# Optimization experiments

Measured on AMD Instinct MI355X. Metric: run time of the kernel, lower is better.

Reference implementation:

```python
import jax, jax.numpy as jnp
import numpy as np

H = 16          # num_attention_heads
HD = 64         # attention_head_size
ALPHA = 1.5
BANDWIDTH = 1.0
A_EXP = 0.5     # sinkhorn-like exponent 'a'
DIST_SCALE = float(HD)  # alpha < 2 => scale by head_size
EPS = 1e-12     # F.normalize eps


def setup_inputs() -> dict:
    key = jax.random.key(0)
    ks = jax.random.split(key, 5)
    B, L, D = 2, 1024, 1024
    w_scale = 0.02  # keep distances in a non-degenerate range for the power-law kernel
    x = jax.random.normal(ks[0], (B, L, D), dtype=jnp.float32)
    WQ = jax.random.normal(ks[1], (D, D), dtype=jnp.float32) * w_scale
    WK = jax.random.normal(ks[2], (D, D), dtype=jnp.float32) * w_scale
    WV = jax.random.normal(ks[3], (D, D), dtype=jnp.float32) * w_scale
    WO = jax.random.normal(ks[4], (D, D), dtype=jnp.float32) * w_scale
    z = jnp.zeros((D,), dtype=jnp.float32)
    return {"x": x, "WQ": WQ, "bQ": z, "WK": WK, "bK": z,
            "WV": WV, "bV": z, "WO": WO, "bO": z}


def _heads(t, B, L):
    # [B, L, H*HD] -> [B, H, L, HD]
    return t.reshape(B, L, H, HD).transpose(0, 2, 1, 3)


def reference(x, WQ, bQ, WK, bK, WV, bV, WO, bO):
    B, L, D = x.shape
    q = _heads(x @ WQ + bQ, B, L)   # [B,H,L,HD]
    k = _heads(x @ WK + bK, B, L)
    v = _heads(x @ WV + bV, B, L)

    # torch.cdist(q, k, p=2): pairwise euclidean distance [B,H,L,L]
    q2 = jnp.sum(q * q, axis=-1)                      # [B,H,L]
    k2 = jnp.sum(k * k, axis=-1)                      # [B,H,L]
    qk = jnp.einsum('bhid,bhjd->bhij', q, k)          # [B,H,L,L]
    d2 = q2[..., :, None] + k2[..., None, :] - 2.0 * qk
    g_dist = jnp.sqrt(jnp.maximum(d2, EPS)) / DIST_SCALE

    # alpha < 2: power-law kernel (1 + g/sqrt(bw))^(-(d_intrinsic + alpha))
    attn_score = (1.0 + g_dist / np.sqrt(BANDWIDTH)) ** (-(HD + ALPHA))

    # a > 0: Sinkhorn-style row/col renormalization
    N_R = jnp.sum(attn_score, axis=-1)                # [B,H,L] row sums
    N_C = jnp.sum(attn_score, axis=-2)                # [B,H,L] col sums
    K_tilde = (N_R ** (-A_EXP))[..., :, None] * attn_score * (N_C ** (-A_EXP))[..., None, :]

    # F.normalize(p=1, dim=3); entries are positive so |.| sum == sum
    attention_probs = K_tilde / jnp.maximum(jnp.sum(K_tilde, axis=-1, keepdims=True), EPS)

    out = jnp.einsum('bhij,bhjd->bhid', attention_probs, v)   # [B,H,L,HD]
    out = out.transpose(0, 2, 1, 3).reshape(B, L, H * HD)
    return out @ WO + bO
```

## Files before the change

### kernel.cpp

```cpp
#include <hip/hip_runtime.h>
#include <math.h>


typedef __attribute__((ext_vector_type(8))) short short8;
typedef __attribute__((ext_vector_type(4))) float f32x4;

__device__ inline unsigned short f2bf(float f) {
  unsigned int u = __float_as_uint(f);
  unsigned int r = (u + 0x7FFFu + ((u >> 16) & 1u)) >> 16;
  return (unsigned short)r;
}
__device__ inline float bf2f(unsigned short s) {
  return __uint_as_float(((unsigned int)s) << 16);
}
__device__ inline float score_fn(float dot, float sq) {
  float d2 = fmaxf(fmaf(-2.f, dot, sq), 1e-12f);
  float sd = __builtin_amdgcn_sqrtf(d2);
  float lg = __builtin_amdgcn_logf(fmaf(sd, 0.015625f, 1.0f));
  return __builtin_amdgcn_exp2f(-65.5f * lg);
}
__device__ inline unsigned int cvtpk(float lo, float hi) {
  unsigned int r;
  asm("v_cvt_pk_bf16_f32 %0, %1, %2" : "=v"(r) : "v"(lo), "v"(hi));
  return r;
}
#define GLD16(lptr, gptr)                                                      \
  __builtin_amdgcn_global_load_lds(                                            \
      (const __attribute__((address_space(1))) void*)(gptr),                   \
      (__attribute__((address_space(3))) void*)(lptr), 16, 0, 0)

__global__ __launch_bounds__(256) void prep(const float* __restrict__ x,
                                            unsigned short* __restrict__ xb,
                                            const float* __restrict__ W0,
                                            const float* __restrict__ W1,
                                            const float* __restrict__ W2,
                                            const float* __restrict__ W3,
                                            unsigned short* __restrict__ T0,
                                            unsigned short* __restrict__ T1,
                                            unsigned short* __restrict__ T2,
                                            unsigned short* __restrict__ T3) {
  __shared__ float T[32][33];
  int bx = blockIdx.x;
  if (bx < 2048) {
    int i = bx * 256 + threadIdx.x;
    float4 v = ((const float4*)x)[i];
    xb[4 * i + 0] = f2bf(v.x);
    xb[4 * i + 1] = f2bf(v.y);
    xb[4 * i + 2] = f2bf(v.z);
    xb[4 * i + 3] = f2bf(v.w);
    return;
  }
  int idx = bx - 2048;
  int z = idx >> 10, rem = idx & 1023;
  const float* W = z == 0 ? W0 : z == 1 ? W1 : z == 2 ? W2 : W3;
  unsigned short* WT = z == 0 ? T0 : z == 1 ? T1 : z == 2 ? T2 : T3;
  int k0 = (rem >> 5) * 32, n0 = (rem & 31) * 32;
  int c = threadIdx.x & 31, r8 = threadIdx.x >> 5;
#pragma unroll
  for (int it = 0; it < 4; ++it) {
    int rr = r8 + it * 8;
    T[rr][c] = W[(size_t)(k0 + rr) * 1024 + n0 + c];
  }
  __syncthreads();
#pragma unroll
  for (int it = 0; it < 4; ++it) {
    int rr = r8 + it * 8;
    WT[(size_t)(n0 + rr) * 1024 + k0 + c] = f2bf(T[c][rr]);
  }
}

__global__ __launch_bounds__(512, 2) void gemm128k64(const unsigned short* __restrict__ A,
                                                     const unsigned short* __restrict__ B0,
                                                     const unsigned short* __restrict__ B1,
                                                     const unsigned short* __restrict__ B2,
                                                     const float* __restrict__ c0,
                                                     const float* __restrict__ c1,
                                                     const float* __restrict__ c2,
                                                     void* __restrict__ Y0,
                                                     void* __restrict__ Y1,
                                                     void* __restrict__ Y2,
                                                     float* __restrict__ sq0,
                                                     float* __restrict__ sq1,
                                                     float* __restrict__ sq2,
                                                     int m0, int m1, int m2) {
  int z = blockIdx.z;
  const unsigned short* BT = z == 0 ? B0 : z == 1 ? B1 : B2;
  const float* bias = z == 0 ? c0 : z == 1 ? c1 : c2;
  void* Y = z == 0 ? Y0 : z == 1 ? Y1 : Y2;
  float* sq = z == 0 ? sq0 : z == 1 ? sq1 : sq2;
  int mode = z == 0 ? m0 : z == 1 ? m1 : m2;

  __shared__ __align__(16) unsigned short As[2][128 * 64];
  __shared__ __align__(16) unsigned short Bs[2][128 * 64];
  int tid = threadIdx.x;
  int w = tid >> 6, l = tid & 63, g = l >> 4, l15 = l & 15;
  int wm = w >> 2, wn = w & 3;
  int bm = blockIdx.x * 128, bn = blockIdx.y * 128;
  const int x7 = l15 & 7;

  const int i0 = tid, i1 = tid + 512;
  const int r0 = i0 >> 3, s0 = (i0 & 7) ^ (r0 & 7);
  const int r1 = i1 >> 3, s1 = (i1 & 7) ^ (r1 & 7);

  GLD16(&As[0][i0 * 8], &A[(size_t)(bm + r0) * 1024 + s0 * 8]);
  GLD16(&As[0][i1 * 8], &A[(size_t)(bm + r1) * 1024 + s1 * 8]);
  GLD16(&Bs[0][i0 * 8], &BT[(size_t)(bn + r0) * 1024 + s0 * 8]);
  GLD16(&Bs[0][i1 * 8], &BT[(size_t)(bn + r1) * 1024 + s1 * 8]);

  f32x4 acc[4][2];
#pragma unroll
  for (int mi = 0; mi < 4; ++mi)
#pragma unroll
    for (int ni = 0; ni < 2; ++ni)
#pragma unroll
      for (int r = 0; r < 4; ++r) acc[mi][ni][r] = 0.f;

  __syncthreads();
  for (int t = 0; t < 16; ++t) {
    int cur = t & 1;
    if (t < 15) {
      int kn = (t + 1) * 64;
      GLD16(&As[cur ^ 1][i0 * 8], &A[(size_t)(bm + r0) * 1024 + kn + s0 * 8]);
      GLD16(&As[cur ^ 1][i1 * 8], &A[(size_t)(bm + r1) * 1024 + kn + s1 * 8]);
      GLD16(&Bs[cur ^ 1][i0 * 8], &BT[(size_t)(bn + r0) * 1024 + kn + s0 * 8]);
      GLD16(&Bs[cur ^ 1][i1 * 8], &BT[(size_t)(bn + r1) * 1024 + kn + s1 * 8]);
    }
#pragma unroll
    for (int kc = 0; kc < 2; ++kc) {
      const int cread = (((kc << 2) + g) ^ x7) * 8;
      short8 a[4], b[2];
#pragma unroll
      for (int mi = 0; mi < 4; ++mi)
        a[mi] = *(const short8*)&As[cur][(wm * 64 + mi * 16 + l15) * 64 + cread];
#pragma unroll
      for (int ni = 0; ni < 2; ++ni)
        b[ni] = *(const short8*)&Bs[cur][(wn * 32 + ni * 16 + l15) * 64 + cread];
#pragma unroll
      for (int mi = 0; mi < 4; ++mi)
#pragma unroll
        for (int ni = 0; ni < 2; ++ni)
          acc[mi][ni] = __builtin_amdgcn_mfma_f32_16x16x32_bf16(a[mi], b[ni], acc[mi][ni], 0, 0, 0);
    }
    __syncthreads();
  }

  float rowsq[4][4];
#pragma unroll
  for (int mi = 0; mi < 4; ++mi)
#pragma unroll
    for (int r = 0; r < 4; ++r) rowsq[mi][r] = 0.f;

#pragma unroll
  for (int ni = 0; ni < 2; ++ni) {
    int n = bn + wn * 32 + ni * 16 + l15;
    float bv = bias[n];
#pragma unroll
    for (int mi = 0; mi < 4; ++mi) {
#pragma unroll
      for (int r = 0; r < 4; ++r) {
        int m = bm + wm * 64 + mi * 16 + 4 * g + r;
        float v = acc[mi][ni][r] + bv;
        if (mode == 0) {
          int b = m >> 10, ll = m & 1023, h = n >> 6, hd = n & 63;
          unsigned short ush = f2bf(v);
          ((unsigned short*)Y)[(((size_t)(b * 16 + h) * 1024) + ll) * 64 + hd] = ush;
          float f = bf2f(ush);
          rowsq[mi][r] = fmaf(f, f, rowsq[mi][r]);
        } else if (mode == 1) {
          int b = m >> 10, ll = m & 1023, h = n >> 6, hd = n & 63;
          int jp = (ll & ~31) | (((ll >> 2) & 3) * 8 + ((ll >> 4) & 1) * 4 + (ll & 3));
          ((unsigned short*)Y)[(((size_t)(b * 16 + h) * 64) + hd) * 1024 + jp] = f2bf(v);
        } else {
          ((float*)Y)[(size_t)m * 1024 + n] = v;
        }
      }
    }
  }

  if (sq != nullptr) {
    float* Sq = (float*)&As[0][0];
#pragma unroll
    for (int mi = 0; mi < 4; ++mi)
#pragma unroll
      for (int r = 0; r < 4; ++r) {
        float s = rowsq[mi][r];
        s += __shfl_xor(s, 1);
        s += __shfl_xor(s, 2);
        s += __shfl_xor(s, 4);
        s += __shfl_xor(s, 8);
        rowsq[mi][r] = s;
      }
    if (l15 == 0) {
#pragma unroll
      for (int mi = 0; mi < 4; ++mi)
#pragma unroll
        for (int r = 0; r < 4; ++r)
          Sq[(wm * 4 + wn) * 64 + mi * 16 + 4 * g + r] = rowsq[mi][r];
    }
    __syncthreads();
    if (tid < 256) {
      int rr = tid & 127, hh = tid >> 7;
      float s = Sq[((rr >> 6) * 4 + 2 * hh) * 64 + (rr & 63)] +
                Sq[((rr >> 6) * 4 + 2 * hh + 1) * 64 + (rr & 63)];
      int m = bm + rr, b = m >> 10, ll = m & 1023;
      int h = (bn >> 6) + hh;
      sq[(size_t)(b * 16 + h) * 1024 + ll] = s;
    }
  }
}

__global__ __launch_bounds__(256) void gemm_st(const unsigned short* __restrict__ A,
                                               const unsigned short* __restrict__ BT,
                                               const float* __restrict__ bias,
                                               float* __restrict__ Y) {
  __shared__ __align__(16) unsigned short As[2][64 * 64];
  __shared__ __align__(16) unsigned short Bs[2][64 * 64];
  int tid = threadIdx.x;
  int w = tid >> 6, l = tid & 63, g = l >> 4, l15 = l & 15;
  int bm = blockIdx.x * 64, bn = blockIdx.y * 64;
  const int arow = w * 16 + l15;
  const int x7 = l15 & 7;

  const int i0s = tid, i1s = 256 + tid;
  const int r0 = i0s >> 3, s0 = (i0s & 7) ^ (r0 & 7);
  const int r1 = i1s >> 3, s1 = (i1s & 7) ^ (r1 & 7);

  GLD16(&As[0][i0s * 8], &A[(size_t)(bm + r0) * 1024 + s0 * 8]);
  GLD16(&As[0][i1s * 8], &A[(size_t)(bm + r1) * 1024 + s1 * 8]);
  GLD16(&Bs[0][i0s * 8], &BT[(size_t)(bn + r0) * 1024 + s0 * 8]);
  GLD16(&Bs[0][i1s * 8], &BT[(size_t)(bn + r1) * 1024 + s1 * 8]);

  f32x4 acc[4];
#pragma unroll
  for (int t = 0; t < 4; ++t)
#pragma unroll
    for (int r = 0; r < 4; ++r) acc[t][r] = 0.f;

  __syncthreads();
  for (int t = 0; t < 16; ++t) {
    int cur = t & 1;
    if (t < 15) {
      int kn = (t + 1) * 64;
      GLD16(&As[cur ^ 1][i0s * 8], &A[(size_t)(bm + r0) * 1024 + kn + s0 * 8]);
      GLD16(&As[cur ^ 1][i1s * 8], &A[(size_t)(bm + r1) * 1024 + kn + s1 * 8]);
      GLD16(&Bs[cur ^ 1][i0s * 8], &BT[(size_t)(bn + r0) * 1024 + kn + s0 * 8]);
      GLD16(&Bs[cur ^ 1][i1s * 8], &BT[(size_t)(bn + r1) * 1024 + kn + s1 * 8]);
    }
#pragma unroll
    for (int kc = 0; kc < 2; ++kc) {
      short8 a = *(const short8*)&As[cur][arow * 64 + ((kc * 4 + g) ^ x7) * 8];
#pragma unroll
      for (int tt = 0; tt < 4; ++tt) {
        short8 b = *(const short8*)&Bs[cur][(tt * 16 + l15) * 64 + ((kc * 4 + g) ^ x7) * 8];
        acc[tt] = __builtin_amdgcn_mfma_f32_16x16x32_bf16(a, b, acc[tt], 0, 0, 0);
      }
    }
    __syncthreads();
  }

#pragma unroll
  for (int t = 0; t < 4; ++t) {
    int n = bn + 16 * t + l15;
    float bv = bias[n];
#pragma unroll
    for (int r = 0; r < 4; ++r) {
      int m = bm + w * 16 + 4 * g + r;
      Y[(size_t)m * 1024 + n] = acc[t][r] + bv;
    }
  }
}

__global__ __launch_bounds__(256, 2) void colsum_mfma(const unsigned short* __restrict__ Qb,
                                                      const unsigned short* __restrict__ Kb,
                                                      const float* __restrict__ q2,
                                                      const float* __restrict__ k2,
                                                      float* __restrict__ rnc) {
  __shared__ __align__(16) unsigned short Qd[2][128 * 64];
  __shared__ __align__(16) float q2s[1024];
  int bh = blockIdx.x, jt = blockIdx.y;
  int tid = threadIdx.x, w = tid >> 6, l = tid & 63;
  int g = l >> 4, l15 = l & 15;
  const int x7 = l15 & 7;
  const unsigned short* Qp = Qb + (size_t)bh * 65536;
  const unsigned short* Kp = Kb + (size_t)bh * 65536;
  int j = jt * 64 + w * 16 + l15;

  int rQ[4], sQ[4];
#pragma unroll
  for (int it = 0; it < 4; ++it) {
    int c = tid + 256 * it;
    rQ[it] = c >> 3;
    sQ[it] = (c & 7) ^ (rQ[it] & 7);
  }

  GLD16(&q2s[tid * 4], q2 + (size_t)bh * 1024 + tid * 4);
#pragma unroll
  for (int it = 0; it < 4; ++it)
    GLD16(&Qd[0][(tid + 256 * it) * 8], Qp + (size_t)rQ[it] * 64 + sQ[it] * 8);

  short8 bk0 = *(const short8*)&Kp[(size_t)j * 64 + 8 * g];
  short8 bk1 = *(const short8*)&Kp[(size_t)j * 64 + 32 + 8 * g];
  float k2j = k2[(size_t)bh * 1024 + j];
  float colacc = 0.f;

  __syncthreads();
  for (int t = 0; t < 8; ++t) {
    int cur = t & 1;
    if (t < 7) {
      int inx = (t + 1) * 128;
#pragma unroll
      for (int it = 0; it < 4; ++it)
        GLD16(&Qd[cur ^ 1][(tid + 256 * it) * 8], Qp + (size_t)(inx + rQ[it]) * 64 + sQ[it] * 8);
    }
    const unsigned short* Ql = Qd[cur];
#pragma unroll
    for (int tp = 0; tp < 8; ++tp) {
      int rowb = (16 * tp + l15) * 64;
      short8 a0 = *(const short8*)&Ql[rowb + ((g) ^ x7) * 8];
      short8 a1 = *(const short8*)&Ql[rowb + ((4 + g) ^ x7) * 8];
      f32x4 cf;
#pragma unroll
      for (int r = 0; r < 4; ++r) cf[r] = 0.f;
      __builtin_amdgcn_s_setprio(1);
      cf = __builtin_amdgcn_mfma_f32_16x16x32_bf16(a0, bk0, cf, 0, 0, 0);
      cf = __builtin_amdgcn_mfma_f32_16x16x32_bf16(a1, bk1, cf, 0, 0, 0);
      __builtin_amdgcn_s_setprio(0);
      float4 qv = *(const float4*)&q2s[t * 128 + 16 * tp + 4 * g];
      colacc += score_fn(cf[0], qv.x + k2j);
      colacc += score_fn(cf[1], qv.y + k2j);
      colacc += score_fn(cf[2], qv.z + k2j);
      colacc += score_fn(cf[3], qv.w + k2j);
    }
    __syncthreads();
  }
  colacc += __shfl_xor(colacc, 16);
  colacc += __shfl_xor(colacc, 32);
  if (l < 16) rnc[(size_t)bh * 1024 + jt * 64 + w * 16 + l] = __builtin_amdgcn_rsqf(colacc);
}

__global__ __launch_bounds__(256, 2) void attn_mfma(const unsigned short* __restrict__ Qb,
                                                    const unsigned short* __restrict__ Kb,
                                                    const unsigned short* __restrict__ VTp,
                                                    const float* __restrict__ q2,
                                                    const float* __restrict__ k2,
                                                    const float* __restrict__ rnc,
                                                    unsigned short* __restrict__ AO) {
  __shared__ __align__(16) unsigned short Kd[2][128 * 64];
  __shared__ __align__(16) unsigned short Vd[2][64 * 128];
  __shared__ __align__(16) float k2s[1024];
  __shared__ __align__(16) float rns[1024];
  int bh = blockIdx.x;
  int tid = threadIdx.x, w = tid >> 6, l = tid & 63;
  int g = l >> 4, l15 = l & 15;
  const int x7 = l15 & 7;
  int it0 = blockIdx.y * 64 + w * 16;
  const unsigned short* Qp = Qb + (size_t)bh * 65536;
  const unsigned short* Kp = Kb + (size_t)bh * 65536;
  const unsigned short* Vp = VTp + (size_t)bh * 65536;
  int b = bh >> 4, h = bh & 15;

  int rK[4], cK[4], rV[4], cV[4];
#pragma unroll
  for (int it = 0; it < 4; ++it) {
    int c = tid + 256 * it;
    rK[it] = c >> 3;
    cK[it] = ((c & 7) ^ (rK[it] & 7));
    rV[it] = c >> 4;
    int s = c & 15;
    cV[it] = (s & 8) | ((s & 7) ^ (rV[it] & 7));
  }

  GLD16(&k2s[tid * 4], k2 + (size_t)bh * 1024 + tid * 4);
  GLD16(&rns[tid * 4], rnc + (size_t)bh * 1024 + tid * 4);
#pragma unroll
  for (int it = 0; it < 4; ++it) {
    GLD16(&Kd[0][(tid + 256 * it) * 8], Kp + (size_t)rK[it] * 64 + cK[it] * 8);
    GLD16(&Vd[0][(tid + 256 * it) * 8], Vp + (size_t)rV[it] * 1024 + cV[it] * 8);
  }

  short8 bq0 = *(const short8*)&Qp[(size_t)(it0 + l15) * 64 + 8 * g];
  short8 bq1 = *(const short8*)&Qp[(size_t)(it0 + l15) * 64 + 32 + 8 * g];
  float q2l = q2[(size_t)bh * 1024 + it0 + l15];

  f32x4 o[4];
#pragma unroll
  for (int t = 0; t < 4; ++t)
#pragma unroll
    for (int r = 0; r < 4; ++r) o[t][r] = 0.f;
  float dacc = 0.f;

  __syncthreads();
  for (int t = 0; t < 8; ++t) {
    int cur = t & 1;
    if (t < 7) {
      int j0n = (t + 1) * 128;
#pragma unroll
      for (int it = 0; it < 4; ++it) {
        GLD16(&Kd[cur ^ 1][(tid + 256 * it) * 8], Kp + (size_t)(j0n + rK[it]) * 64 + cK[it] * 8);
        GLD16(&Vd[cur ^ 1][(tid + 256 * it) * 8], Vp + (size_t)rV[it] * 1024 + j0n + cV[it] * 8);
      }
    }
    const unsigned short* Kl = Kd[cur];
    const unsigned short* Vl = Vd[cur];
#pragma unroll
    for (int jj = 0; jj < 2; ++jj) {
      float sc[16];
#pragma unroll
      for (int tp = 0; tp < 4; ++tp) {
        int rowb = (jj * 64 + 16 * tp + l15) * 64;
        short8 a0 = *(const short8*)&Kl[rowb + ((g) ^ x7) * 8];
        short8 a1 = *(const short8*)&Kl[rowb + ((4 + g) ^ x7) * 8];
        f32x4 cf;
#pragma unroll
        for (int r = 0; r < 4; ++r) cf[r] = 0.f;
        __builtin_amdgcn_s_setprio(1);
        cf = __builtin_amdgcn_mfma_f32_16x16x32_bf16(a0, bq0, cf, 0, 0, 0);
        cf = __builtin_amdgcn_mfma_f32_16x16x32_bf16(a1, bq1, cf, 0, 0, 0);
        __builtin_amdgcn_s_setprio(0);
        int base = t * 128 + jj * 64 + 16 * tp + 4 * g;
        float4 kv = *(const float4*)&k2s[base];
        float4 rv = *(const float4*)&rns[base];
        sc[tp * 4 + 0] = score_fn(cf[0], q2l + kv.x) * rv.x;
        sc[tp * 4 + 1] = score_fn(cf[1], q2l + kv.y) * rv.y;
        sc[tp * 4 + 2] = score_fn(cf[2], q2l + kv.z) * rv.z;
        sc[tp * 4 + 3] = score_fn(cf[3], q2l + kv.w) * rv.w;
      }
#pragma unroll
      for (int i = 0; i < 16; ++i) dacc += sc[i];
      int pi0[4], pi1[4];
      pi0[0] = (int)cvtpk(sc[0], sc[1]);
      pi0[1] = (int)cvtpk(sc[2], sc[3]);
      pi0[2] = (int)cvtpk(sc[4], sc[5]);
      pi0[3] = (int)cvtpk(sc[6], sc[7]);
      pi1[0] = (int)cvtpk(sc[8], sc[9]);
      pi1[1] = (int)cvtpk(sc[10], sc[11]);
      pi1[2] = (int)cvtpk(sc[12], sc[13]);
      pi1[3] = (int)cvtpk(sc[14], sc[15]);
      short8 pa0 = *(short8*)pi0;
      short8 pa1 = *(short8*)pi1;
#pragma unroll
      for (int t5 = 0; t5 < 4; ++t5) {
        int vr = 16 * t5 + l15;
        short8 bv0 = *(const short8*)&Vl[vr * 128 + (jj * 8 + ((g) ^ x7)) * 8];
        short8 bv1 = *(const short8*)&Vl[vr * 128 + (jj * 8 + ((4 + g) ^ x7)) * 8];
        __builtin_amdgcn_s_setprio(1);
        o[t5] = __builtin_amdgcn_mfma_f32_16x16x32_bf16(pa0, bv0, o[t5], 0, 0, 0);
        o[t5] = __builtin_amdgcn_mfma_f32_16x16x32_bf16(pa1, bv1, o[t5], 0, 0, 0);
        __builtin_amdgcn_s_setprio(0);
      }
    }
    __syncthreads();
  }

  dacc += __shfl_xor(dacc, 16);
  dacc += __shfl_xor(dacc, 32);
  float dv[4];
#pragma unroll
  for (int r = 0; r < 4; ++r) dv[r] = __shfl(dacc, 4 * g + r);

#pragma unroll
  for (int t = 0; t < 4; ++t) {
#pragma unroll
    for (int r = 0; r < 4; ++r) {
      int m = b * 1024 + it0 + 4 * g + r;
      int n = h * 64 + t * 16 + l15;
      AO[(size_t)m * 1024 + n] = f2bf(o[t][r] / dv[r]);
    }
  }
}

extern "C" void kernel_launch(void* const* d_in, const int* in_sizes, int n_in,
                              void* d_out, int out_size, void* d_ws, size_t ws_size,
                              hipStream_t stream) {
  const float* x  = (const float*)d_in[0];
  const float* WQ = (const float*)d_in[1];
  const float* bQ = (const float*)d_in[2];
  const float* WK = (const float*)d_in[3];
  const float* bK = (const float*)d_in[4];
  const float* WV = (const float*)d_in[5];
  const float* bV = (const float*)d_in[6];
  const float* WO = (const float*)d_in[7];
  const float* bO = (const float*)d_in[8];

  char* base = (char*)d_ws;
  unsigned short* xb  = (unsigned short*)(base);
  unsigned short* WQT = (unsigned short*)(base + (4u  << 20));
  unsigned short* WKT = (unsigned short*)(base + (6u  << 20));
  unsigned short* WVT = (unsigned short*)(base + (8u  << 20));
  unsigned short* WOT = (unsigned short*)(base + (10u << 20));
  unsigned short* Qb  = (unsigned short*)(base + (12u << 20));
  unsigned short* Kb  = (unsigned short*)(base + (16u << 20));
  unsigned short* VTp = (unsigned short*)(base + (20u << 20));
  unsigned short* AOb = (unsigned short*)(base + (24u << 20));
  float* q2  = (float*)(base + (28u << 20));
  float* k2  = (float*)(base + (28u << 20) + (128u << 10));
  float* rnc = (float*)(base + (28u << 20) + (256u << 10));

  prep<<<6144, 256, 0, stream>>>(x, xb, WQ, WK, WV, WO, WQT, WKT, WVT, WOT);

  gemm128k64<<<dim3(16, 8, 3), 512, 0, stream>>>(xb, WQT, WKT, WVT, bQ, bK, bV,
                                                 Qb, Kb, VTp, q2, k2, nullptr,
                                                 0, 0, 1);

  colsum_mfma<<<dim3(32, 16), 256, 0, stream>>>(Qb, Kb, q2, k2, rnc);
  attn_mfma<<<dim3(32, 16), 256, 0, stream>>>(Qb, Kb, VTp, q2, k2, rnc, AOb);

  gemm_st<<<dim3(32, 16), 256, 0, stream>>>(AOb, WOT, bO, (float*)d_out);
}
```

Baseline: 98.72 us.

## Split colsum and attention over the key/query dimension with a combine pass

The column-sum and attention kernels are each split in two along the reduction dimension (grid z=2), so twice as many blocks run with smaller LDS tiles and a higher occupancy hint. Partial column sums are added and turned into inverse square roots inside the attention kernel. Partial outputs and row denominators go to fp32 workspace, and a new combine kernel sums them, normalizes and writes bf16. The aim is to fill the 256 CUs better than 512 blocks could, at the cost of an extra launch and extra global traffic for the fp32 partials.

```diff
diff --git a/kernel.cpp b/kernel.cpp
--- a/kernel.cpp
+++ b/kernel.cpp
@@ -270,33 +270,29 @@
   }
 }
 
-__global__ __launch_bounds__(256, 2) void colsum_mfma(const unsigned short* __restrict__ Qb,
+__global__ __launch_bounds__(256, 4) void colsum_part(const unsigned short* __restrict__ Qb,
                                                       const unsigned short* __restrict__ Kb,
                                                       const float* __restrict__ q2,
                                                       const float* __restrict__ k2,
-                                                      float* __restrict__ rnc) {
-  __shared__ __align__(16) unsigned short Qd[2][128 * 64];
-  __shared__ __align__(16) float q2s[1024];
-  int bh = blockIdx.x, jt = blockIdx.y;
+                                                      float* __restrict__ ncp) {
+  __shared__ __align__(16) unsigned short Qd[2][64 * 64];
+  __shared__ __align__(16) float q2s[512];
+  int bh = blockIdx.x, jt = blockIdx.y, ih = blockIdx.z;
   int tid = threadIdx.x, w = tid >> 6, l = tid & 63;
   int g = l >> 4, l15 = l & 15;
   const int x7 = l15 & 7;
   const unsigned short* Qp = Qb + (size_t)bh * 65536;
   const unsigned short* Kp = Kb + (size_t)bh * 65536;
+  const int ibase = ih * 512;
   int j = jt * 64 + w * 16 + l15;
 
-  int rQ[4], sQ[4];
-#pragma unroll
-  for (int it = 0; it < 4; ++it) {
-    int c = tid + 256 * it;
-    rQ[it] = c >> 3;
-    sQ[it] = (c & 7) ^ (rQ[it] & 7);
-  }
-
-  GLD16(&q2s[tid * 4], q2 + (size_t)bh * 1024 + tid * 4);
-#pragma unroll
-  for (int it = 0; it < 4; ++it)
-    GLD16(&Qd[0][(tid + 256 * it) * 8], Qp + (size_t)rQ[it] * 64 + sQ[it] * 8);
+  const int i0s = tid, i1s = 256 + tid;
+  const int r0 = i0s >> 3, s0 = (i0s & 7) ^ (r0 & 7);
+  const int r1 = i1s >> 3, s1 = (i1s & 7) ^ (r1 & 7);
+
+  if (tid < 128) GLD16(&q2s[tid * 4], q2 + (size_t)bh * 1024 + ibase + tid * 4);
+  GLD16(&Qd[0][i0s * 8], Qp + (size_t)(ibase + r0) * 64 + s0 * 8);
+  GLD16(&Qd[0][i1s * 8], Qp + (size_t)(ibase + r1) * 64 + s1 * 8);
 
   short8 bk0 = *(const short8*)&Kp[(size_t)j * 64 + 8 * g];
   short8 bk1 = *(const short8*)&Kp[(size_t)j * 64 + 32 + 8 * g];
@@ -307,14 +303,13 @@
   for (int t = 0; t < 8; ++t) {
     int cur = t & 1;
     if (t < 7) {
-      int inx = (t + 1) * 128;
-#pragma unroll
-      for (int it = 0; it < 4; ++it)
-        GLD16(&Qd[cur ^ 1][(tid + 256 * it) * 8], Qp + (size_t)(inx + rQ[it]) * 64 + sQ[it] * 8);
+      int inx = ibase + (t + 1) * 64;
+      GLD16(&Qd[cur ^ 1][i0s * 8], Qp + (size_t)(inx + r0) * 64 + s0 * 8);
+      GLD16(&Qd[cur ^ 1][i1s * 8], Qp + (size_t)(inx + r1) * 64 + s1 * 8);
     }
     const unsigned short* Ql = Qd[cur];
 #pragma unroll
-    for (int tp = 0; tp < 8; ++tp) {
+    for (int tp = 0; tp < 4; ++tp) {
       int rowb = (16 * tp + l15) * 64;
       short8 a0 = *(const short8*)&Ql[rowb + ((g) ^ x7) * 8];
       short8 a1 = *(const short8*)&Ql[rowb + ((4 + g) ^ x7) * 8];
@@ -325,7 +320,7 @@
       cf = __builtin_amdgcn_mfma_f32_16x16x32_bf16(a0, bk0, cf, 0, 0, 0);
       cf = __builtin_amdgcn_mfma_f32_16x16x32_bf16(a1, bk1, cf, 0, 0, 0);
       __builtin_amdgcn_s_setprio(0);
-      float4 qv = *(const float4*)&q2s[t * 128 + 16 * tp + 4 * g];
+      float4 qv = *(const float4*)&q2s[t * 64 + 16 * tp + 4 * g];
       colacc += score_fn(cf[0], qv.x + k2j);
       colacc += score_fn(cf[1], qv.y + k2j);
       colacc += score_fn(cf[2], qv.z + k2j);
@@ -335,48 +330,50 @@
   }
   colacc += __shfl_xor(colacc, 16);
   colacc += __shfl_xor(colacc, 32);
-  if (l < 16) rnc[(size_t)bh * 1024 + jt * 64 + w * 16 + l] = __builtin_amdgcn_rsqf(colacc);
-}
-
-__global__ __launch_bounds__(256, 2) void attn_mfma(const unsigned short* __restrict__ Qb,
+  if (l < 16)
+    ncp[(size_t)(ih * 32 + bh) * 1024 + jt * 64 + w * 16 + l] = colacc;
+}
+
+__global__ __launch_bounds__(256, 4) void attn_part(const unsigned short* __restrict__ Qb,
                                                     const unsigned short* __restrict__ Kb,
                                                     const unsigned short* __restrict__ VTp,
                                                     const float* __restrict__ q2,
                                                     const float* __restrict__ k2,
-                                                    const float* __restrict__ rnc,
-                                                    unsigned short* __restrict__ AO) {
-  __shared__ __align__(16) unsigned short Kd[2][128 * 64];
-  __shared__ __align__(16) unsigned short Vd[2][64 * 128];
-  __shared__ __align__(16) float k2s[1024];
-  __shared__ __align__(16) float rns[1024];
-  int bh = blockIdx.x;
+                                                    const float* __restrict__ ncp,
+                                                    float* __restrict__ Opart,
+                                                    float* __restrict__ dpart) {
+  __shared__ __align__(16) unsigned short Kd[2][64 * 64];
+  __shared__ __align__(16) unsigned short Vd[2][64 * 64];
+  __shared__ __align__(16) float k2s[512];
+  __shared__ __align__(16) float rns[512];
+  int bh = blockIdx.x, it = blockIdx.y, jh = blockIdx.z;
   int tid = threadIdx.x, w = tid >> 6, l = tid & 63;
   int g = l >> 4, l15 = l & 15;
   const int x7 = l15 & 7;
-  int it0 = blockIdx.y * 64 + w * 16;
+  int it0 = it * 64 + w * 16;
+  const int jg = jh * 512;
   const unsigned short* Qp = Qb + (size_t)bh * 65536;
   const unsigned short* Kp = Kb + (size_t)bh * 65536;
   const unsigned short* Vp = VTp + (size_t)bh * 65536;
-  int b = bh >> 4, h = bh & 15;
-
-  int rK[4], cK[4], rV[4], cV[4];
-#pragma unroll
-  for (int it = 0; it < 4; ++it) {
-    int c = tid + 256 * it;
-    rK[it] = c >> 3;
-    cK[it] = ((c & 7) ^ (rK[it] & 7));
-    rV[it] = c >> 4;
-    int s = c & 15;
-    cV[it] = (s & 8) | ((s & 7) ^ (rV[it] & 7));
-  }
-
-  GLD16(&k2s[tid * 4], k2 + (size_t)bh * 1024 + tid * 4);
-  GLD16(&rns[tid * 4], rnc + (size_t)bh * 1024 + tid * 4);
-#pragma unroll
-  for (int it = 0; it < 4; ++it) {
-    GLD16(&Kd[0][(tid + 256 * it) * 8], Kp + (size_t)rK[it] * 64 + cK[it] * 8);
-    GLD16(&Vd[0][(tid + 256 * it) * 8], Vp + (size_t)rV[it] * 1024 + cV[it] * 8);
-  }
+
+  {
+    float2 a0 = *(const float2*)&ncp[(size_t)bh * 1024 + jg + tid * 2];
+    float2 a1 = *(const float2*)&ncp[(size_t)(32 + bh) * 1024 + jg + tid * 2];
+    rns[tid * 2 + 0] = __builtin_amdgcn_rsqf(a0.x + a1.x);
+    rns[tid * 2 + 1] = __builtin_amdgcn_rsqf(a0.y + a1.y);
+    float2 kk = *(const float2*)&k2[(size_t)bh * 1024 + jg + tid * 2];
+    k2s[tid * 2 + 0] = kk.x;
+    k2s[tid * 2 + 1] = kk.y;
+  }
+
+  const int i0s = tid, i1s = 256 + tid;
+  const int r0 = i0s >> 3, s0 = (i0s & 7) ^ (r0 & 7);
+  const int r1 = i1s >> 3, s1 = (i1s & 7) ^ (r1 & 7);
+
+  GLD16(&Kd[0][i0s * 8], Kp + (size_t)(jg + r0) * 64 + s0 * 8);
+  GLD16(&Kd[0][i1s * 8], Kp + (size_t)(jg + r1) * 64 + s1 * 8);
+  GLD16(&Vd[0][i0s * 8], Vp + (size_t)r0 * 1024 + jg + s0 * 8);
+  GLD16(&Vd[0][i1s * 8], Vp + (size_t)r1 * 1024 + jg + s1 * 8);
 
   short8 bq0 = *(const short8*)&Qp[(size_t)(it0 + l15) * 64 + 8 * g];
   short8 bq1 = *(const short8*)&Qp[(size_t)(it0 + l15) * 64 + 32 + 8 * g];
@@ -393,79 +390,106 @@
   for (int t = 0; t < 8; ++t) {
     int cur = t & 1;
     if (t < 7) {
-      int j0n = (t + 1) * 128;
-#pragma unroll
-      for (int it = 0; it < 4; ++it) {
-        GLD16(&Kd[cur ^ 1][(tid + 256 * it) * 8], Kp + (size_t)(j0n + rK[it]) * 64 + cK[it] * 8);
-        GLD16(&Vd[cur ^ 1][(tid + 256 * it) * 8], Vp + (size_t)rV[it] * 1024 + j0n + cV[it] * 8);
-      }
+      int j0n = jg + (t + 1) * 64;
+      GLD16(&Kd[cur ^ 1][i0s * 8], Kp + (size_t)(j0n + r0) * 64 + s0 * 8);
+      GLD16(&Kd[cur ^ 1][i1s * 8], Kp + (size_t)(j0n + r1) * 64 + s1 * 8);
+      GLD16(&Vd[cur ^ 1][i0s * 8], Vp + (size_t)r0 * 1024 + j0n + s0 * 8);
+      GLD16(&Vd[cur ^ 1][i1s * 8], Vp + (size_t)r1 * 1024 + j0n + s1 * 8);
     }
     const unsigned short* Kl = Kd[cur];
     const unsigned short* Vl = Vd[cur];
-#pragma unroll
-    for (int jj = 0; jj < 2; ++jj) {
-      float sc[16];
-#pragma unroll
-      for (int tp = 0; tp < 4; ++tp) {
-        int rowb = (jj * 64 + 16 * tp + l15) * 64;
-        short8 a0 = *(const short8*)&Kl[rowb + ((g) ^ x7) * 8];
-        short8 a1 = *(const short8*)&Kl[rowb + ((4 + g) ^ x7) * 8];
-        f32x4 cf;
-#pragma unroll
-        for (int r = 0; r < 4; ++r) cf[r] = 0.f;
-        __builtin_amdgcn_s_setprio(1);
-        cf = __builtin_amdgcn_mfma_f32_16x16x32_bf16(a0, bq0, cf, 0, 0, 0);
-        cf = __builtin_amdgcn_mfma_f32_16x16x32_bf16(a1, bq1, cf, 0, 0, 0);
-        __builtin_amdgcn_s_setprio(0);
-        int base = t * 128 + jj * 64 + 16 * tp + 4 * g;
-        float4 kv = *(const float4*)&k2s[base];
-        float4 rv = *(const float4*)&rns[base];
-        sc[tp * 4 + 0] = score_fn(cf[0], q2l + kv.x) * rv.x;
-        sc[tp * 4 + 1] = score_fn(cf[1], q2l + kv.y) * rv.y;
-        sc[tp * 4 + 2] = score_fn(cf[2], q2l + kv.z) * rv.z;
-        sc[tp * 4 + 3] = score_fn(cf[3], q2l + kv.w) * rv.w;
-      }
-#pragma unroll
-      for (int i = 0; i < 16; ++i) dacc += sc[i];
-      int pi0[4], pi1[4];
-      pi0[0] = (int)cvtpk(sc[0], sc[1]);
-      pi0[1] = (int)cvtpk(sc[2], sc[3]);
-      pi0[2] = (int)cvtpk(sc[4], sc[5]);
-      pi0[3] = (int)cvtpk(sc[6], sc[7]);
-      pi1[0] = (int)cvtpk(sc[8], sc[9]);
-      pi1[1] = (int)cvtpk(sc[10], sc[11]);
-      pi1[2] = (int)cvtpk(sc[12], sc[13]);
-      pi1[3] = (int)cvtpk(sc[14], sc[15]);
-      short8 pa0 = *(short8*)pi0;
-      short8 pa1 = *(short8*)pi1;
-#pragma unroll
-      for (int t5 = 0; t5 < 4; ++t5) {
-        int vr = 16 * t5 + l15;
-        short8 bv0 = *(const short8*)&Vl[vr * 128 + (jj * 8 + ((g) ^ x7)) * 8];
-        short8 bv1 = *(const short8*)&Vl[vr * 128 + (jj * 8 + ((4 + g) ^ x7)) * 8];
-        __builtin_amdgcn_s_setprio(1);
-        o[t5] = __builtin_amdgcn_mfma_f32_16x16x32_bf16(pa0, bv0, o[t5], 0, 0, 0);
-        o[t5] = __builtin_amdgcn_mfma_f32_16x16x32_bf16(pa1, bv1, o[t5], 0, 0, 0);
-        __builtin_amdgcn_s_setprio(0);
-      }
+    float sc[16];
+#pragma unroll
+    for (int tp = 0; tp < 4; ++tp) {
+      int rowb = (16 * tp + l15) * 64;
+      short8 a0 = *(const short8*)&Kl[rowb + ((g) ^ x7) * 8];
+      short8 a1 = *(const short8*)&Kl[rowb + ((4 + g) ^ x7) * 8];
+      f32x4 cf;
+#pragma unroll
+      for (int r = 0; r < 4; ++r) cf[r] = 0.f;
+      __builtin_amdgcn_s_setprio(1);
+      cf = __builtin_amdgcn_mfma_f32_16x16x32_bf16(a0, bq0, cf, 0, 0, 0);
+      cf = __builtin_amdgcn_mfma_f32_16x16x32_bf16(a1, bq1, cf, 0, 0, 0);
+      __builtin_amdgcn_s_setprio(0);
+      int base = t * 64 + 16 * tp + 4 * g;
+      float4 kv = *(const float4*)&k2s[base];
+      float4 rv = *(const float4*)&rns[base];
+      sc[tp * 4 + 0] = score_fn(cf[0], q2l + kv.x) * rv.x;
+      sc[tp * 4 + 1] = score_fn(cf[1], q2l + kv.y) * rv.y;
+      sc[tp * 4 + 2] = score_fn(cf[2], q2l + kv.z) * rv.z;
+      sc[tp * 4 + 3] = score_fn(cf[3], q2l + kv.w) * rv.w;
+    }
+#pragma unroll
+    for (int i = 0; i < 16; ++i) dacc += sc[i];
+    int pi0[4], pi1[4];
+    pi0[0] = (int)cvtpk(sc[0], sc[1]);
+    pi0[1] = (int)cvtpk(sc[2], sc[3]);
+    pi0[2] = (int)cvtpk(sc[4], sc[5]);
+    pi0[3] = (int)cvtpk(sc[6], sc[7]);
+    pi1[0] = (int)cvtpk(sc[8], sc[9]);
+    pi1[1] = (int)cvtpk(sc[10], sc[11]);
+    pi1[2] = (int)cvtpk(sc[12], sc[13]);
+    pi1[3] = (int)cvtpk(sc[14], sc[15]);
+    short8 pa0 = *(short8*)pi0;
+    short8 pa1 = *(short8*)pi1;
+#pragma unroll
+    for (int t5 = 0; t5 < 4; ++t5) {
+      int rowb = (16 * t5 + l15) * 64;
+      short8 v0 = *(const short8*)&Vl[rowb + ((g) ^ x7) * 8];
+      short8 v1 = *(const short8*)&Vl[rowb + ((4 + g) ^ x7) * 8];
+      __builtin_amdgcn_s_setprio(1);
+      o[t5] = __builtin_amdgcn_mfma_f32_16x16x32_bf16(pa0, v0, o[t5], 0, 0, 0);
+      o[t5] = __builtin_amdgcn_mfma_f32_16x16x32_bf16(pa1, v1, o[t5], 0, 0, 0);
+      __builtin_amdgcn_s_setprio(0);
     }
     __syncthreads();
   }
 
   dacc += __shfl_xor(dacc, 16);
   dacc += __shfl_xor(dacc, 32);
-  float dv[4];
-#pragma unroll
-  for (int r = 0; r < 4; ++r) dv[r] = __shfl(dacc, 4 * g + r);
-
-#pragma unroll
-  for (int t = 0; t < 4; ++t) {
+  if (l < 16)
+    dpart[(size_t)(jh * 32 + bh) * 1024 + it * 64 + w * 16 + l] = dacc;
+
+  float* Ob = Opart + ((size_t)(jh * 32 + bh) * 16 + it) * 4096;
+#pragma unroll
+  for (int t5 = 0; t5 < 4; ++t5) {
 #pragma unroll
     for (int r = 0; r < 4; ++r) {
-      int m = b * 1024 + it0 + 4 * g + r;
-      int n = h * 64 + t * 16 + l15;
-      AO[(size_t)m * 1024 + n] = f2bf(o[t][r] / dv[r]);
-    }
+      int ri = w * 16 + 4 * g + r;
+      int ci = 16 * t5 + l15;
+      Ob[ri * 64 + ci] = o[t5][r];
+    }
+  }
+}
+
+__global__ __launch_bounds__(256) void combine(const float* __restrict__ Opart,
+                                               const float* __restrict__ dpart,
+                                               unsigned short* __restrict__ AO) {
+  __shared__ float dl[64];
+  int bh = blockIdx.x, it = blockIdx.y;
+  int tid = threadIdx.x;
+  int b = bh >> 4, h = bh & 15;
+  const float* O0 = Opart + ((size_t)bh * 16 + it) * 4096;
+  const float* O1 = Opart + ((size_t)(32 + bh) * 16 + it) * 4096;
+  if (tid < 64)
+    dl[tid] = dpart[(size_t)bh * 1024 + it * 64 + tid] +
+              dpart[(size_t)(32 + bh) * 1024 + it * 64 + tid];
+  __syncthreads();
+#pragma unroll
+  for (int e = 0; e < 4; ++e) {
+    int idx = (tid + e * 256) * 4;
+    int ri = idx >> 6, ci = idx & 63;
+    float4 a = *(const float4*)&O0[idx];
+    float4 c = *(const float4*)&O1[idx];
+    float inv = 1.0f / dl[ri];
+    unsigned short outv[4];
+    outv[0] = f2bf((a.x + c.x) * inv);
+    outv[1] = f2bf((a.y + c.y) * inv);
+    outv[2] = f2bf((a.z + c.z) * inv);
+    outv[3] = f2bf((a.w + c.w) * inv);
+    int m = b * 1024 + it * 64 + ri;
+    int n = h * 64 + ci;
+    *(unsigned long long*)&AO[(size_t)m * 1024 + n] = *(unsigned long long*)outv;
   }
 }
 
@@ -492,9 +516,11 @@
   unsigned short* Kb  = (unsigned short*)(base + (16u << 20));
   unsigned short* VTp = (unsigned short*)(base + (20u << 20));
   unsigned short* AOb = (unsigned short*)(base + (24u << 20));
-  float* q2  = (float*)(base + (28u << 20));
-  float* k2  = (float*)(base + (28u << 20) + (128u << 10));
-  float* rnc = (float*)(base + (28u << 20) + (256u << 10));
+  float* q2    = (float*)(base + (28u << 20));
+  float* k2    = (float*)(base + (28u << 20) + (128u << 10));
+  float* ncp   = (float*)(base + (29u << 20));
+  float* dpart = (float*)(base + (30u << 20));
+  float* Opart = (float*)(base + (31u << 20));
 
   prep<<<6144, 256, 0, stream>>>(x, xb, WQ, WK, WV, WO, WQT, WKT, WVT, WOT);
 
@@ -502,8 +528,10 @@
                                                  Qb, Kb, VTp, q2, k2, nullptr,
                                                  0, 0, 1);
 
-  colsum_mfma<<<dim3(32, 16), 256, 0, stream>>>(Qb, Kb, q2, k2, rnc);
-  attn_mfma<<<dim3(32, 16), 256, 0, stream>>>(Qb, Kb, VTp, q2, k2, rnc, AOb);
+  colsum_part<<<dim3(32, 16, 2), 256, 0, stream>>>(Qb, Kb, q2, k2, ncp);
+  attn_part<<<dim3(32, 16, 2), 256, 0, stream>>>(Qb, Kb, VTp, q2, k2, ncp,
+                                                 Opart, dpart);
+  combine<<<dim3(32, 16), 256, 0, stream>>>(Opart, dpart, AOb);
 
   gemm_st<<<dim3(32, 16), 256, 0, stream>>>(AOb, WOT, bO, (float*)d_out);
 }
```

Result: slower. 102.2 us (+3.5%).

## Materialize score matrix once and fold column normalization into scaled V

Applied to the files above, without the earlier changes.

Before, the power-law score matrix was computed twice: once to get column sums and again inside the attention kernel. Now a first pass computes the scores once, writes them as a bf16 matrix P to global memory, and accumulates column sums. A small kernel then scales V by the inverse square root of those sums and appends a row of those factors, so the P·V pass also yields the row denominators. This removes the duplicate transcendental work but adds about 64 MB of P writes and reads plus an extra launch, and the column scaling is now applied after bf16 rounding of the unscaled scores.

```diff
diff --git a/kernel.cpp b/kernel.cpp
--- a/kernel.cpp
+++ b/kernel.cpp
@@ -270,201 +270,215 @@
   }
 }
 
-__global__ __launch_bounds__(256, 2) void colsum_mfma(const unsigned short* __restrict__ Qb,
-                                                      const unsigned short* __restrict__ Kb,
-                                                      const float* __restrict__ q2,
-                                                      const float* __restrict__ k2,
-                                                      float* __restrict__ rnc) {
-  __shared__ __align__(16) unsigned short Qd[2][128 * 64];
+__global__ __launch_bounds__(256, 4) void passA(const unsigned short* __restrict__ Qb,
+                                                const unsigned short* __restrict__ Kb,
+                                                const float* __restrict__ q2,
+                                                const float* __restrict__ k2,
+                                                unsigned short* __restrict__ P,
+                                                float* __restrict__ rnc) {
+  __shared__ __align__(16) unsigned short Qd[2][64 * 64];
   __shared__ __align__(16) float q2s[1024];
+  __shared__ __align__(16) unsigned int Pb[2][64][36];
+  __shared__ float colred[4][64];
   int bh = blockIdx.x, jt = blockIdx.y;
   int tid = threadIdx.x, w = tid >> 6, l = tid & 63;
   int g = l >> 4, l15 = l & 15;
   const int x7 = l15 & 7;
   const unsigned short* Qp = Qb + (size_t)bh * 65536;
   const unsigned short* Kp = Kb + (size_t)bh * 65536;
-  int j = jt * 64 + w * 16 + l15;
-
-  int rQ[4], sQ[4];
-#pragma unroll
-  for (int it = 0; it < 4; ++it) {
-    int c = tid + 256 * it;
-    rQ[it] = c >> 3;
-    sQ[it] = (c & 7) ^ (rQ[it] & 7);
-  }
+
+  const int i0s = tid, i1s = 256 + tid;
+  const int r0 = i0s >> 3, s0 = (i0s & 7) ^ (r0 & 7);
+  const int r1 = i1s >> 3, s1 = (i1s & 7) ^ (r1 & 7);
 
   GLD16(&q2s[tid * 4], q2 + (size_t)bh * 1024 + tid * 4);
-#pragma unroll
-  for (int it = 0; it < 4; ++it)
-    GLD16(&Qd[0][(tid + 256 * it) * 8], Qp + (size_t)rQ[it] * 64 + sQ[it] * 8);
-
-  short8 bk0 = *(const short8*)&Kp[(size_t)j * 64 + 8 * g];
-  short8 bk1 = *(const short8*)&Kp[(size_t)j * 64 + 32 + 8 * g];
-  float k2j = k2[(size_t)bh * 1024 + j];
-  float colacc = 0.f;
+  GLD16(&Qd[0][i0s * 8], Qp + (size_t)r0 * 64 + s0 * 8);
+  GLD16(&Qd[0][i1s * 8], Qp + (size_t)r1 * 64 + s1 * 8);
+
+  short8 ak[4][2];
+#pragma unroll
+  for (int tp = 0; tp < 4; ++tp) {
+#pragma unroll
+    for (int hf = 0; hf < 2; ++hf)
+      ak[tp][hf] = *(const short8*)&Kp[(size_t)(jt * 64 + 16 * tp + l15) * 64 + hf * 32 + 8 * g];
+  }
+  float k2v[16];
+#pragma unroll
+  for (int tp = 0; tp < 4; ++tp) {
+    float4 kk = *(const float4*)&k2[(size_t)bh * 1024 + jt * 64 + 16 * tp + 4 * g];
+    k2v[tp * 4 + 0] = kk.x; k2v[tp * 4 + 1] = kk.y;
+    k2v[tp * 4 + 2] = kk.z; k2v[tp * 4 + 3] = kk.w;
+  }
+  float colpart[16];
+#pragma unroll
+  for (int q = 0; q < 16; ++q) colpart[q] = 0.f;
+
+  const int iloc = w * 16 + l15;
+  const int pr0 = tid >> 3, pc0 = tid & 7;
+  const int pr1 = (tid + 256) >> 3, pc1 = tid & 7;
 
   __syncthreads();
-  for (int t = 0; t < 8; ++t) {
+  for (int t = 0; t < 16; ++t) {
     int cur = t & 1;
-    if (t < 7) {
-      int inx = (t + 1) * 128;
-#pragma unroll
-      for (int it = 0; it < 4; ++it)
-        GLD16(&Qd[cur ^ 1][(tid + 256 * it) * 8], Qp + (size_t)(inx + rQ[it]) * 64 + sQ[it] * 8);
-    }
-    const unsigned short* Ql = Qd[cur];
-#pragma unroll
-    for (int tp = 0; tp < 8; ++tp) {
-      int rowb = (16 * tp + l15) * 64;
-      short8 a0 = *(const short8*)&Ql[rowb + ((g) ^ x7) * 8];
-      short8 a1 = *(const short8*)&Ql[rowb + ((4 + g) ^ x7) * 8];
+    if (t < 15) {
+      int inx = (t + 1) * 64;
+      GLD16(&Qd[cur ^ 1][i0s * 8], Qp + (size_t)(inx + r0) * 64 + s0 * 8);
+      GLD16(&Qd[cur ^ 1][i1s * 8], Qp + (size_t)(inx + r1) * 64 + s1 * 8);
+    }
+    int rowb = iloc * 64;
+    short8 bq0 = *(const short8*)&Qd[cur][rowb + ((g) ^ x7) * 8];
+    short8 bq1 = *(const short8*)&Qd[cur][rowb + ((4 + g) ^ x7) * 8];
+    float q2l = q2s[t * 64 + iloc];
+
+    float sc[16];
+#pragma unroll
+    for (int tp = 0; tp < 4; ++tp) {
       f32x4 cf;
 #pragma unroll
       for (int r = 0; r < 4; ++r) cf[r] = 0.f;
-      __builtin_amdgcn_s_setprio(1);
-      cf = __builtin_amdgcn_mfma_f32_16x16x32_bf16(a0, bk0, cf, 0, 0, 0);
-      cf = __builtin_amdgcn_mfma_f32_16x16x32_bf16(a1, bk1, cf, 0, 0, 0);
-      __builtin_amdgcn_s_setprio(0);
-      float4 qv = *(const float4*)&q2s[t * 128 + 16 * tp + 4 * g];
-      colacc += score_fn(cf[0], qv.x + k2j);
-      colacc += score_fn(cf[1], qv.y + k2j);
-      colacc += score_fn(cf[2], qv.z + k2j);
-      colacc += score_fn(cf[3], qv.w + k2j);
+      cf = __builtin_amdgcn_mfma_f32_16x16x32_bf16(ak[tp][0], bq0, cf, 0, 0, 0);
+      cf = __builtin_amdgcn_mfma_f32_16x16x32_bf16(ak[tp][1], bq1, cf, 0, 0, 0);
+#pragma unroll
+      for (int r = 0; r < 4; ++r)
+        sc[tp * 4 + r] = score_fn(cf[r], q2l + k2v[tp * 4 + r]);
+    }
+#pragma unroll
+    for (int q = 0; q < 16; ++q) colpart[q] += sc[q];
+
+#pragma unroll
+    for (int tp = 0; tp < 4; ++tp) {
+#pragma unroll
+      for (int rp = 0; rp < 2; ++rp) {
+        int dwidx = 16 * (tp >> 1) + 4 * g + 2 * (tp & 1) + rp;
+        Pb[cur][iloc][dwidx] = cvtpk(sc[tp * 4 + 2 * rp], sc[tp * 4 + 2 * rp + 1]);
+      }
     }
     __syncthreads();
-  }
-  colacc += __shfl_xor(colacc, 16);
-  colacc += __shfl_xor(colacc, 32);
-  if (l < 16) rnc[(size_t)bh * 1024 + jt * 64 + w * 16 + l] = __builtin_amdgcn_rsqf(colacc);
-}
-
-__global__ __launch_bounds__(256, 2) void attn_mfma(const unsigned short* __restrict__ Qb,
-                                                    const unsigned short* __restrict__ Kb,
-                                                    const unsigned short* __restrict__ VTp,
-                                                    const float* __restrict__ q2,
-                                                    const float* __restrict__ k2,
-                                                    const float* __restrict__ rnc,
-                                                    unsigned short* __restrict__ AO) {
-  __shared__ __align__(16) unsigned short Kd[2][128 * 64];
-  __shared__ __align__(16) unsigned short Vd[2][64 * 128];
-  __shared__ __align__(16) float k2s[1024];
-  __shared__ __align__(16) float rns[1024];
-  int bh = blockIdx.x;
+    {
+      short8 v0 = *(const short8*)((const char*)&Pb[cur][0][0] + 144 * pr0 + 16 * pc0);
+      short8 v1 = *(const short8*)((const char*)&Pb[cur][0][0] + 144 * pr1 + 16 * pc1);
+      *(short8*)&P[((size_t)bh * 1024 + t * 64 + pr0) * 1024 + jt * 64 + 8 * pc0] = v0;
+      *(short8*)&P[((size_t)bh * 1024 + t * 64 + pr1) * 1024 + jt * 64 + 8 * pc1] = v1;
+    }
+  }
+
+#pragma unroll
+  for (int q = 0; q < 16; ++q) {
+    float v = colpart[q];
+    v += __shfl_xor(v, 1);
+    v += __shfl_xor(v, 2);
+    v += __shfl_xor(v, 4);
+    v += __shfl_xor(v, 8);
+    colpart[q] = v;
+  }
+  if (l15 == 0) {
+#pragma unroll
+    for (int q = 0; q < 16; ++q)
+      colred[w][16 * (q >> 2) + 4 * g + (q & 3)] = colpart[q];
+  }
+  __syncthreads();
+  if (tid < 64) {
+    float s = colred[0][tid] + colred[1][tid] + colred[2][tid] + colred[3][tid];
+    rnc[(size_t)bh * 1024 + jt * 64 + tid] = __builtin_amdgcn_rsqf(s);
+  }
+}
+
+__global__ __launch_bounds__(256) void vscale(const unsigned short* __restrict__ VTp,
+                                              const float* __restrict__ rnc,
+                                              unsigned short* __restrict__ Vs) {
+  int bh = blockIdx.x, row = blockIdx.y;
+  int j4 = threadIdx.x * 4;
+  unsigned short out[4];
+#pragma unroll
+  for (int e = 0; e < 4; ++e) {
+    int jp = j4 + e;
+    int p = jp & 31;
+    int gg = (p >> 3) & 3, jj = (p >> 2) & 1, rr = p & 3;
+    int jtrue = (jp & ~31) | (16 * jj + 4 * gg + rr);
+    float rv = rnc[(size_t)bh * 1024 + jtrue];
+    if (row < 64) {
+      float v = bf2f(VTp[((size_t)bh * 64 + row) * 1024 + jp]);
+      out[e] = f2bf(v * rv);
+    } else if (row == 64) {
+      out[e] = f2bf(rv);
+    } else {
+      out[e] = 0;
+    }
+  }
+  *(unsigned long long*)&Vs[((size_t)bh * 80 + row) * 1024 + j4] = *(unsigned long long*)out;
+}
+
+__global__ __launch_bounds__(256, 4) void passB(const unsigned short* __restrict__ P,
+                                                const unsigned short* __restrict__ Vs,
+                                                unsigned short* __restrict__ AO) {
+  __shared__ __align__(16) unsigned short Pd[2][64 * 64];
+  __shared__ __align__(16) unsigned short Vd[2][80 * 64];
+  int bh = blockIdx.x, it = blockIdx.y;
   int tid = threadIdx.x, w = tid >> 6, l = tid & 63;
   int g = l >> 4, l15 = l & 15;
   const int x7 = l15 & 7;
-  int it0 = blockIdx.y * 64 + w * 16;
-  const unsigned short* Qp = Qb + (size_t)bh * 65536;
-  const unsigned short* Kp = Kb + (size_t)bh * 65536;
-  const unsigned short* Vp = VTp + (size_t)bh * 65536;
+  const unsigned short* Pp = P + (size_t)bh * 1048576;
+  const unsigned short* Vp = Vs + (size_t)bh * 81920;
   int b = bh >> 4, h = bh & 15;
 
-  int rK[4], cK[4], rV[4], cV[4];
-#pragma unroll
-  for (int it = 0; it < 4; ++it) {
-    int c = tid + 256 * it;
-    rK[it] = c >> 3;
-    cK[it] = ((c & 7) ^ (rK[it] & 7));
-    rV[it] = c >> 4;
-    int s = c & 15;
-    cV[it] = (s & 8) | ((s & 7) ^ (rV[it] & 7));
-  }
-
-  GLD16(&k2s[tid * 4], k2 + (size_t)bh * 1024 + tid * 4);
-  GLD16(&rns[tid * 4], rnc + (size_t)bh * 1024 + tid * 4);
-#pragma unroll
-  for (int it = 0; it < 4; ++it) {
-    GLD16(&Kd[0][(tid + 256 * it) * 8], Kp + (size_t)rK[it] * 64 + cK[it] * 8);
-    GLD16(&Vd[0][(tid + 256 * it) * 8], Vp + (size_t)rV[it] * 1024 + cV[it] * 8);
-  }
-
-  short8 bq0 = *(const short8*)&Qp[(size_t)(it0 + l15) * 64 + 8 * g];
-  short8 bq1 = *(const short8*)&Qp[(size_t)(it0 + l15) * 64 + 32 + 8 * g];
-  float q2l = q2[(size_t)bh * 1024 + it0 + l15];
-
-  f32x4 o[4];
-#pragma unroll
-  for (int t = 0; t < 4; ++t)
-#pragma unroll
-    for (int r = 0; r < 4; ++r) o[t][r] = 0.f;
-  float dacc = 0.f;
+  const int cP0 = tid, cP1 = tid + 256;
+  const int rP0 = cP0 >> 3, sP0 = (cP0 & 7) ^ (rP0 & 7);
+  const int rP1 = cP1 >> 3, sP1 = (cP1 & 7) ^ (rP1 & 7);
+  const int cV0 = tid, cV1 = tid + 256, cV2 = tid + 512;
+  const int rV0 = cV0 >> 3, sV0 = (cV0 & 7) ^ (rV0 & 7);
+  const int rV1 = cV1 >> 3, sV1 = (cV1 & 7) ^ (rV1 & 7);
+  const int rV2 = cV2 >> 3, sV2 = (cV2 & 7) ^ (rV2 & 7);
+
+  GLD16(&Pd[0][cP0 * 8], Pp + (size_t)(it * 64 + rP0) * 1024 + sP0 * 8);
+  GLD16(&Pd[0][cP1 * 8], Pp + (size_t)(it * 64 + rP1) * 1024 + sP1 * 8);
+  GLD16(&Vd[0][cV0 * 8], Vp + (size_t)rV0 * 1024 + sV0 * 8);
+  GLD16(&Vd[0][cV1 * 8], Vp + (size_t)rV1 * 1024 + sV1 * 8);
+  if (tid < 128) GLD16(&Vd[0][cV2 * 8], Vp + (size_t)rV2 * 1024 + sV2 * 8);
+
+  f32x4 o[5];
+#pragma unroll
+  for (int t5 = 0; t5 < 5; ++t5)
+#pragma unroll
+    for (int r = 0; r < 4; ++r) o[t5][r] = 0.f;
 
   __syncthreads();
-  for (int t = 0; t < 8; ++t) {
+  for (int t = 0; t < 16; ++t) {
     int cur = t & 1;
-    if (t < 7) {
-      int j0n = (t + 1) * 128;
-#pragma unroll
-      for (int it = 0; it < 4; ++it) {
-        GLD16(&Kd[cur ^ 1][(tid + 256 * it) * 8], Kp + (size_t)(j0n + rK[it]) * 64 + cK[it] * 8);
-        GLD16(&Vd[cur ^ 1][(tid + 256 * it) * 8], Vp + (size_t)rV[it] * 1024 + j0n + cV[it] * 8);
-      }
-    }
-    const unsigned short* Kl = Kd[cur];
-    const unsigned short* Vl = Vd[cur];
-#pragma unroll
-    for (int jj = 0; jj < 2; ++jj) {
-      float sc[16];
-#pragma unroll
-      for (int tp = 0; tp < 4; ++tp) {
-        int rowb = (jj * 64 + 16 * tp + l15) * 64;
-        short8 a0 = *(const short8*)&Kl[rowb + ((g) ^ x7) * 8];
-        short8 a1 = *(const short8*)&Kl[rowb + ((4 + g) ^ x7) * 8];
-        f32x4 cf;
-#pragma unroll
-        for (int r = 0; r < 4; ++r) cf[r] = 0.f;
-        __builtin_amdgcn_s_setprio(1);
-        cf = __builtin_amdgcn_mfma_f32_16x16x32_bf16(a0, bq0, cf, 0, 0, 0);
-        cf = __builtin_amdgcn_mfma_f32_16x16x32_bf16(a1, bq1, cf, 0, 0, 0);
-        __builtin_amdgcn_s_setprio(0);
-        int base = t * 128 + jj * 64 + 16 * tp + 4 * g;
-        float4 kv = *(const float4*)&k2s[base];
-        float4 rv = *(const float4*)&rns[base];
-        sc[tp * 4 + 0] = score_fn(cf[0], q2l + kv.x) * rv.x;
-        sc[tp * 4 + 1] = score_fn(cf[1], q2l + kv.y) * rv.y;
-        sc[tp * 4 + 2] = score_fn(cf[2], q2l + kv.z) * rv.z;
-        sc[tp * 4 + 3] = score_fn(cf[3], q2l + kv.w) * rv.w;
-      }
-#pragma unroll
-      for (int i = 0; i < 16; ++i) dacc += sc[i];
-      int pi0[4], pi1[4];
-      pi0[0] = (int)cvtpk(sc[0], sc[1]);
-      pi0[1] = (int)cvtpk(sc[2], sc[3]);
-      pi0[2] = (int)cvtpk(sc[4], sc[5]);
-      pi0[3] = (int)cvtpk(sc[6], sc[7]);
-      pi1[0] = (int)cvtpk(sc[8], sc[9]);
-      pi1[1] = (int)cvtpk(sc[10], sc[11]);
-      pi1[2] = (int)cvtpk(sc[12], sc[13]);
-      pi1[3] = (int)cvtpk(sc[14], sc[15]);
-      short8 pa0 = *(short8*)pi0;
-      short8 pa1 = *(short8*)pi1;
-#pragma unroll
-      for (int t5 = 0; t5 < 4; ++t5) {
-        int vr = 16 * t5 + l15;
-        short8 bv0 = *(const short8*)&Vl[vr * 128 + (jj * 8 + ((g) ^ x7)) * 8];
-        short8 bv1 = *(const short8*)&Vl[vr * 128 + (jj * 8 + ((4 + g) ^ x7)) * 8];
-        __builtin_amdgcn_s_setprio(1);
-        o[t5] = __builtin_amdgcn_mfma_f32_16x16x32_bf16(pa0, bv0, o[t5], 0, 0, 0);
-        o[t5] = __builtin_amdgcn_mfma_f32_16x16x32_bf16(pa1, bv1, o[t5], 0, 0, 0);
-        __builtin_amdgcn_s_setprio(0);
-      }
+    if (t < 15) {
+      int jn = (t + 1) * 64;
+      GLD16(&Pd[cur ^ 1][cP0 * 8], Pp + (size_t)(it * 64 + rP0) * 1024 + jn + sP0 * 8);
+      GLD16(&Pd[cur ^ 1][cP1 * 8], Pp + (size_t)(it * 64 + rP1) * 1024 + jn + sP1 * 8);
+      GLD16(&Vd[cur ^ 1][cV0 * 8], Vp + (size_t)rV0 * 1024 + jn + sV0 * 8);
+      GLD16(&Vd[cur ^ 1][cV1 * 8], Vp + (size_t)rV1 * 1024 + jn + sV1 * 8);
+      if (tid < 128) GLD16(&Vd[cur ^ 1][cV2 * 8], Vp + (size_t)rV2 * 1024 + jn + sV2 * 8);
+    }
+    int rowb = (w * 16 + l15) * 64;
+    short8 pa0 = *(const short8*)&Pd[cur][rowb + ((g) ^ x7) * 8];
+    short8 pa1 = *(const short8*)&Pd[cur][rowb + ((4 + g) ^ x7) * 8];
+#pragma unroll
+    for (int t5 = 0; t5 < 5; ++t5) {
+      int vrow = (16 * t5 + l15) * 64;
+      short8 bv0 = *(const short8*)&Vd[cur][vrow + ((g) ^ x7) * 8];
+      short8 bv1 = *(const short8*)&Vd[cur][vrow + ((4 + g) ^ x7) * 8];
+      __builtin_amdgcn_s_setprio(1);
+      o[t5] = __builtin_amdgcn_mfma_f32_16x16x32_bf16(pa0, bv0, o[t5], 0, 0, 0);
+      o[t5] = __builtin_amdgcn_mfma_f32_16x16x32_bf16(pa1, bv1, o[t5], 0, 0, 0);
+      __builtin_amdgcn_s_setprio(0);
     }
     __syncthreads();
   }
 
-  dacc += __shfl_xor(dacc, 16);
-  dacc += __shfl_xor(dacc, 32);
   float dv[4];
 #pragma unroll
-  for (int r = 0; r < 4; ++r) dv[r] = __shfl(dacc, 4 * g + r);
-
-#pragma unroll
-  for (int t = 0; t < 4; ++t) {
+  for (int r = 0; r < 4; ++r) dv[r] = __shfl(o[4][r], 16 * g);
+
+#pragma unroll
+  for (int t5 = 0; t5 < 4; ++t5) {
 #pragma unroll
     for (int r = 0; r < 4; ++r) {
-      int m = b * 1024 + it0 + 4 * g + r;
-      int n = h * 64 + t * 16 + l15;
-      AO[(size_t)m * 1024 + n] = f2bf(o[t][r] / dv[r]);
+      int m = b * 1024 + it * 64 + w * 16 + 4 * g + r;
+      int n = h * 64 + 16 * t5 + l15;
+      AO[(size_t)m * 1024 + n] = f2bf(o[t5][r] / dv[r]);
     }
   }
 }
@@ -495,6 +509,8 @@
   float* q2  = (float*)(base + (28u << 20));
   float* k2  = (float*)(base + (28u << 20) + (128u << 10));
   float* rnc = (float*)(base + (28u << 20) + (256u << 10));
+  unsigned short* Vs = (unsigned short*)(base + (30u << 20));
+  unsigned short* P  = (unsigned short*)(base + (36u << 20));
 
   prep<<<6144, 256, 0, stream>>>(x, xb, WQ, WK, WV, WO, WQT, WKT, WVT, WOT);
 
@@ -502,8 +518,9 @@
                                                  Qb, Kb, VTp, q2, k2, nullptr,
                                                  0, 0, 1);
 
-  colsum_mfma<<<dim3(32, 16), 256, 0, stream>>>(Qb, Kb, q2, k2, rnc);
-  attn_mfma<<<dim3(32, 16), 256, 0, stream>>>(Qb, Kb, VTp, q2, k2, rnc, AOb);
+  passA<<<dim3(32, 16), 256, 0, stream>>>(Qb, Kb, q2, k2, P, rnc);
+  vscale<<<dim3(32, 80), 256, 0, stream>>>(VTp, rnc, Vs);
+  passB<<<dim3(32, 16), 256, 0, stream>>>(P, Vs, AOb);
 
   gemm_st<<<dim3(32, 16), 256, 0, stream>>>(AOb, WOT, bO, (float*)d_out);
 }
```

After: 103.6 us. 1.05x slower.
